# Kernel optimization log

Measured on AMD Instinct MI355X. Metric: run time of the kernel, lower is better.

## Reference

```python
import jax, jax.numpy as jnp
import numpy as np

B, S, E, H, L, V = 4, 1024, 256, 512, 16, 8000


def setup_inputs() -> dict:
    key = jax.random.key(0)
    ks = jax.random.split(key, 8)
    return {
        "sent": jax.random.randint(ks[0], (B, S), 0, V),
        "mask": jax.random.randint(ks[1], (B, S), 0, 2),
        "char_emb_w": jax.random.normal(ks[2], (V, E), dtype=jnp.float32) * 0.02,
        "mask_emb_w": jax.random.normal(ks[3], (2, E), dtype=jnp.float32) * 0.02,
        "wA": jax.random.normal(ks[4], (E, H), dtype=jnp.float32) * (1.0 / np.sqrt(E)),
        "bA": jnp.zeros((H,), dtype=jnp.float32),
        "wB": jax.random.normal(ks[5], (E, H), dtype=jnp.float32) * (1.0 / np.sqrt(E)),
        "bB": jnp.zeros((H,), dtype=jnp.float32),
        "wS": jax.random.normal(ks[6], (E, L), dtype=jnp.float32) * (1.0 / np.sqrt(E)),
        "bS": jnp.zeros((L,), dtype=jnp.float32),
    }


def reference(sent, mask, char_emb_w, mask_emb_w, wA, bA, wB, bB, wS, bS):
    # Embedding lookups: (B,S,E)
    ce = char_emb_w[sent]
    me = mask_emb_w[mask]
    # vemb = char_emb * GELU(mask_emb)  (torch GELU default = exact erf form)
    vemb = ce * jax.nn.gelu(me, approximate=False)
    va = vemb @ wA + bA                      # (B,S,H)
    vb = jax.nn.sigmoid(vemb @ wB + bB)      # (B,S,H)
    vc = jnp.einsum("bih,bjh->bij", va, vb) / H   # (B,S,S), biaffine score
    vd = jax.nn.relu(vemb @ wS + bS)         # (B,S,L)
    # torch: matmul(vc.unsqueeze(3), vd.unsqueeze(2)) -> (B,S,S,L) rank-1 outer product
    pred = jax.nn.softmax(vc[..., None] * vd[:, :, None, :], axis=-1)
    return pred
```

## Files before the change

kernel.cpp:

```cpp
#include <hip/hip_runtime.h>
#include <hip/hip_bf16.h>
#include <math.h>

typedef __attribute__((ext_vector_type(8))) short short8;
typedef __attribute__((ext_vector_type(4))) float f32x4;
typedef unsigned short u16;

#define Sn 1024
#define En 256
#define Hn 512
#define Ln 16

__device__ inline u16 bf16b(float x) {
    union { __hip_bfloat16 h; u16 u; } cvt;
    cvt.h = __float2bfloat16(x);
    return cvt.u;
}

__global__ void prep_embed(const float* __restrict__ wA, const float* __restrict__ wB,
                           const float* __restrict__ wS, u16* __restrict__ Wt,
                           const int* __restrict__ sent, const int* __restrict__ mask,
                           const float* __restrict__ ce_w, const float* __restrict__ me_w,
                           u16* __restrict__ vemb) {
    int bx = blockIdx.x;
    if (bx < 1088) {
        int idx = bx * 256 + threadIdx.x;
        int n = idx >> 8;
        int k = idx & 255;
        float v = 0.f;
        if (n < 512)       v = wA[k * 512 + n];
        else if (n < 1024) v = wB[k * 512 + (n - 512)];
        else if (n < 1040) v = wS[k * 16 + (n - 1024)];
        Wt[idx] = bf16b(v);
    } else {
        int row = bx - 1088;
        int e = threadIdx.x;
        int s = sent[row];
        int m = mask[row];
        float ce = ce_w[s * En + e];
        float me = me_w[m * En + e];
        float g = 0.5f * me * (1.f + erff(me * 0.70710678118654752f));
        vemb[row * En + e] = bf16b(ce * g);
    }
}

#define LDP 136
__global__ __launch_bounds__(256, 2) void gemm1(const u16* __restrict__ A, const u16* __restrict__ Bt,
                                                const float* __restrict__ bA, const float* __restrict__ bB,
                                                const float* __restrict__ bS,
                                                u16* __restrict__ va, u16* __restrict__ vb,
                                                float* __restrict__ vd,
                                                float* __restrict__ dmn, float* __restrict__ dmx) {
    __shared__ __align__(16) u16 As[64 * LDP];
    __shared__ __align__(16) u16 Bs[64 * LDP];
    int tid = threadIdx.x;
    int m0 = blockIdx.x * 64, n0 = blockIdx.y * 64;
    int lane = tid & 63, w = tid >> 6;
    int lrow = lane & 15, quad = lane >> 4;

    f32x4 acc[4];
    for (int nt = 0; nt < 4; nt++) acc[nt] = (f32x4){0.f, 0.f, 0.f, 0.f};

    for (int kb = 0; kb < 2; kb++) {
        for (int i = 0; i < 4; i++) {
            int off = (i * 256 + tid) * 8;
            int r = off >> 7, c = off & 127;
            *(short8*)&As[r * LDP + c] = *(const short8*)&A[(m0 + r) * 256 + kb * 128 + c];
            *(short8*)&Bs[r * LDP + c] = *(const short8*)&Bt[(n0 + r) * 256 + kb * 128 + c];
        }
        __syncthreads();
        for (int ks = 0; ks < 4; ks++) {
            short8 a = *(const short8*)&As[(w * 16 + lrow) * LDP + ks * 32 + quad * 8];
            for (int nt = 0; nt < 4; nt++) {
                short8 b = *(const short8*)&Bs[(nt * 16 + lrow) * LDP + ks * 32 + quad * 8];
                acc[nt] = __builtin_amdgcn_mfma_f32_16x16x32_bf16(a, b, acc[nt], 0, 0, 0);
            }
        }
        __syncthreads();
    }
    int mbase = m0 + w * 16 + quad * 4;
    if (blockIdx.y < 8) {
        for (int nt = 0; nt < 4; nt++) {
            int n = n0 + nt * 16 + lrow;
            float bias = bA[n];
            for (int r = 0; r < 4; r++)
                va[(mbase + r) * 512 + n] = bf16b(acc[nt][r] + bias);
        }
    } else if (blockIdx.y < 16) {
        for (int nt = 0; nt < 4; nt++) {
            int n = n0 + nt * 16 + lrow - 512;
            float bias = bB[n];
            for (int r = 0; r < 4; r++) {
                float x = acc[nt][r] + bias;
                vb[(mbase + r) * 512 + n] = bf16b(1.f / (1.f + __expf(-x)));
            }
        }
    } else {
        float bias = bS[lrow];
        for (int r = 0; r < 4; r++) {
            float x = acc[0][r] + bias;
            x = x > 0.f ? x : 0.f;
            vd[(mbase + r) * 16 + lrow] = x;
            float mn = x, mx = x;
            for (int d = 1; d < 16; d <<= 1) {
                mn = fminf(mn, __shfl_xor(mn, d));
                mx = fmaxf(mx, __shfl_xor(mx, d));
            }
            if (lrow == 0) {
                dmn[mbase + r] = mn;
                dmx[mbase + r] = mx;
            }
        }
    }
}

__global__ __launch_bounds__(256, 2) void gemm2(const u16* __restrict__ va_g, const u16* __restrict__ vb_g,
                                                float* __restrict__ vc) {
    __shared__ __align__(16) u16 As[64 * LDP];
    __shared__ __align__(16) u16 Bs[64 * LDP];
    int tid = threadIdx.x;
    int b = blockIdx.z;
    int m0 = blockIdx.x * 64, n0 = blockIdx.y * 64;
    const u16* A  = va_g + (size_t)b * 1024 * 512;
    const u16* Bt = vb_g + (size_t)b * 1024 * 512;
    int lane = tid & 63, w = tid >> 6;
    int lrow = lane & 15, quad = lane >> 4;

    f32x4 acc[4];
    for (int nt = 0; nt < 4; nt++) acc[nt] = (f32x4){0.f, 0.f, 0.f, 0.f};

    for (int kb = 0; kb < 4; kb++) {
        for (int i = 0; i < 4; i++) {
            int off = (i * 256 + tid) * 8;
            int r = off >> 7, c = off & 127;
            *(short8*)&As[r * LDP + c] = *(const short8*)&A[(m0 + r) * 512 + kb * 128 + c];
            *(short8*)&Bs[r * LDP + c] = *(const short8*)&Bt[(n0 + r) * 512 + kb * 128 + c];
        }
        __syncthreads();
        for (int ks = 0; ks < 4; ks++) {
            short8 a = *(const short8*)&As[(w * 16 + lrow) * LDP + ks * 32 + quad * 8];
            for (int nt = 0; nt < 4; nt++) {
                short8 bfr = *(const short8*)&Bs[(nt * 16 + lrow) * LDP + ks * 32 + quad * 8];
                acc[nt] = __builtin_amdgcn_mfma_f32_16x16x32_bf16(a, bfr, acc[nt], 0, 0, 0);
            }
        }
        __syncthreads();
    }
    const float invH = 1.0f / 512.0f;
    float* C = vc + (size_t)b * 1024 * 1024;
    int mbase = m0 + w * 16 + quad * 4;
    for (int nt = 0; nt < 4; nt++) {
        int n = n0 + nt * 16 + lrow;
        for (int r = 0; r < 4; r++)
            C[(mbase + r) * 1024 + n] = acc[nt][r] * invH;
    }
}

__global__ __launch_bounds__(256) void expand(const float* __restrict__ vc, const float* __restrict__ vd,
                                              const float* __restrict__ dmn, const float* __restrict__ dmx,
                                              float* __restrict__ out) {
    int gid = blockIdx.x * 256 + threadIdx.x;
    int t = gid & 3;
    int grp = gid >> 2;
    int j = grp & 1023;
    int bi = grp >> 10;
    int b = bi >> 10;
    float c = __builtin_nontemporal_load(&vc[grp]);
    int rowd = b * 1024 + j;
    f32x4 d = *(const f32x4*)&vd[rowd * 16 + t * 4];
    float m = (c >= 0.f) ? c * dmx[rowd] : c * dmn[rowd];
    float e0 = __expf(c * d.x - m);
    float e1 = __expf(c * d.y - m);
    float e2 = __expf(c * d.z - m);
    float e3 = __expf(c * d.w - m);
    float s = e0 + e1 + e2 + e3;
    s += __shfl_xor(s, 1);
    s += __shfl_xor(s, 2);
    float inv = 1.f / s;
    f32x4 o;
    o.x = e0 * inv; o.y = e1 * inv; o.z = e2 * inv; o.w = e3 * inv;
    __builtin_nontemporal_store(o, (f32x4*)&out[(size_t)grp * 16 + t * 4]);
}

extern "C" void kernel_launch(void* const* d_in, const int* in_sizes, int n_in,
                              void* d_out, int out_size, void* d_ws, size_t ws_size,
                              hipStream_t stream) {
    const int*   sent = (const int*)d_in[0];
    const int*   mask = (const int*)d_in[1];
    const float* ce_w = (const float*)d_in[2];
    const float* me_w = (const float*)d_in[3];
    const float* wA   = (const float*)d_in[4];
    const float* bA   = (const float*)d_in[5];
    const float* wB   = (const float*)d_in[6];
    const float* bB   = (const float*)d_in[7];
    const float* wS   = (const float*)d_in[8];
    const float* bS   = (const float*)d_in[9];
    float* out = (float*)d_out;

    char* ws = (char*)d_ws;
    u16* vemb = (u16*)ws;  ws += (size_t)4096 * 256 * 2;
    u16* Wt   = (u16*)ws;  ws += (size_t)1088 * 256 * 2;
    u16* va   = (u16*)ws;  ws += (size_t)4096 * 512 * 2;
    u16* vb   = (u16*)ws;  ws += (size_t)4096 * 512 * 2;
    float* vd  = (float*)ws;  ws += (size_t)4096 * 16 * 4;
    float* dmn = (float*)ws;  ws += (size_t)4096 * 4;
    float* dmx = (float*)ws;  ws += (size_t)4096 * 4;
    float* vc  = (float*)ws;  ws += (size_t)4 * 1024 * 1024 * 4;

    prep_embed<<<5184, 256, 0, stream>>>(wA, wB, wS, Wt, sent, mask, ce_w, me_w, vemb);
    gemm1<<<dim3(64, 17), 256, 0, stream>>>(vemb, Wt, bA, bB, bS, va, vb, vd, dmn, dmx);
    gemm2<<<dim3(16, 16, 4), 256, 0, stream>>>(va, vb, vc);
    expand<<<65536, 256, 0, stream>>>(vc, vd, dmn, dmx, out);
}
```

Measured before the change: 306.3 us.

## Fuse biaffine GEMM with rank-1 softmax expansion via shared-memory tile

The second GEMM now stages its 64x64 score tile in shared memory, reusing the operand buffers, and each block writes the softmax-expanded output for that tile directly. This removes the separate expand kernel and the 16 MB round trip of the fp32 score matrix through global memory. The trade-off is a longer GEMM epilogue: only 1024 blocks write the 256 MB output, so there is less parallelism for the store-bound phase than the old 65536-block expand kernel had.

```diff
diff --git a/kernel.cpp b/kernel.cpp
--- a/kernel.cpp
+++ b/kernel.cpp
@@ -114,10 +114,17 @@
     }
 }
 
-__global__ __launch_bounds__(256, 2) void gemm2(const u16* __restrict__ va_g, const u16* __restrict__ vb_g,
-                                                float* __restrict__ vc) {
-    __shared__ __align__(16) u16 As[64 * LDP];
-    __shared__ __align__(16) u16 Bs[64 * LDP];
+__global__ __launch_bounds__(256, 2) void gemm2_softmax(const u16* __restrict__ va_g,
+                                                        const u16* __restrict__ vb_g,
+                                                        const float* __restrict__ vd,
+                                                        const float* __restrict__ dmn,
+                                                        const float* __restrict__ dmx,
+                                                        float* __restrict__ out) {
+    __shared__ __align__(16) u16 smem[2 * 64 * LDP];
+    u16* As = smem;
+    u16* Bs = smem + 64 * LDP;
+    float* vcs = (float*)smem;
+
     int tid = threadIdx.x;
     int b = blockIdx.z;
     int m0 = blockIdx.x * 64, n0 = blockIdx.y * 64;
@@ -146,40 +153,37 @@
         }
         __syncthreads();
     }
+
     const float invH = 1.0f / 512.0f;
-    float* C = vc + (size_t)b * 1024 * 1024;
-    int mbase = m0 + w * 16 + quad * 4;
+    int rbase = w * 16 + quad * 4;
     for (int nt = 0; nt < 4; nt++) {
-        int n = n0 + nt * 16 + lrow;
+        int cl = nt * 16 + lrow;
         for (int r = 0; r < 4; r++)
-            C[(mbase + r) * 1024 + n] = acc[nt][r] * invH;
-    }
-}
-
-__global__ __launch_bounds__(256) void expand(const float* __restrict__ vc, const float* __restrict__ vd,
-                                              const float* __restrict__ dmn, const float* __restrict__ dmx,
-                                              float* __restrict__ out) {
-    int gid = blockIdx.x * 256 + threadIdx.x;
-    int t = gid & 3;
-    int grp = gid >> 2;
-    int j = grp & 1023;
-    int bi = grp >> 10;
-    int b = bi >> 10;
-    float c = __builtin_nontemporal_load(&vc[grp]);
-    int rowd = b * 1024 + j;
-    f32x4 d = *(const f32x4*)&vd[rowd * 16 + t * 4];
-    float m = (c >= 0.f) ? c * dmx[rowd] : c * dmn[rowd];
-    float e0 = __expf(c * d.x - m);
-    float e1 = __expf(c * d.y - m);
-    float e2 = __expf(c * d.z - m);
-    float e3 = __expf(c * d.w - m);
-    float s = e0 + e1 + e2 + e3;
-    s += __shfl_xor(s, 1);
-    s += __shfl_xor(s, 2);
-    float inv = 1.f / s;
-    f32x4 o;
-    o.x = e0 * inv; o.y = e1 * inv; o.z = e2 * inv; o.w = e3 * inv;
-    __builtin_nontemporal_store(o, (f32x4*)&out[(size_t)grp * 16 + t * 4]);
+            vcs[(rbase + r) * 65 + cl] = acc[nt][r] * invH;
+    }
+    __syncthreads();
+
+    int jl = tid >> 2;
+    int t4 = (tid & 3) * 4;
+    int rowd = b * 1024 + n0 + jl;
+    f32x4 d = *(const f32x4*)&vd[rowd * 16 + t4];
+    float mn = dmn[rowd], mx = dmx[rowd];
+    float* obase = out + (((size_t)(b * 1024 + m0) * 1024 + n0 + jl) * 16 + t4);
+    for (int il = 0; il < 64; il++) {
+        float c = vcs[il * 65 + jl];
+        float mval = (c >= 0.f) ? c * mx : c * mn;
+        float e0 = __expf(c * d.x - mval);
+        float e1 = __expf(c * d.y - mval);
+        float e2 = __expf(c * d.z - mval);
+        float e3 = __expf(c * d.w - mval);
+        float s = e0 + e1 + e2 + e3;
+        s += __shfl_xor(s, 1);
+        s += __shfl_xor(s, 2);
+        float inv = 1.f / s;
+        f32x4 o;
+        o.x = e0 * inv; o.y = e1 * inv; o.z = e2 * inv; o.w = e3 * inv;
+        __builtin_nontemporal_store(o, (f32x4*)(obase + (size_t)il * 1024 * 16));
+    }
 }
 
 extern "C" void kernel_launch(void* const* d_in, const int* in_sizes, int n_in,
@@ -205,10 +209,8 @@
     float* vd  = (float*)ws;  ws += (size_t)4096 * 16 * 4;
     float* dmn = (float*)ws;  ws += (size_t)4096 * 4;
     float* dmx = (float*)ws;  ws += (size_t)4096 * 4;
-    float* vc  = (float*)ws;  ws += (size_t)4 * 1024 * 1024 * 4;
 
     prep_embed<<<5184, 256, 0, stream>>>(wA, wB, wS, Wt, sent, mask, ce_w, me_w, vemb);
     gemm1<<<dim3(64, 17), 256, 0, stream>>>(vemb, Wt, bA, bB, bS, va, vb, vd, dmn, dmx);
-    gemm2<<<dim3(16, 16, 4), 256, 0, stream>>>(va, vb, vc);
-    expand<<<65536, 256, 0, stream>>>(vc, vd, dmn, dmx, out);
-}
+    gemm2_softmax<<<dim3(16, 16, 4), 256, 0, stream>>>(va, vb, vd, dmn, dmx, out);
+}
```

Result: no change. 308.3 us (+0.7%).

## Retile biaffine GEMM to 128x128 per block and store scores as bf16

Applied to the files above, without the earlier changes.

The batched va·vbᵀ GEMM moves from 64x64 tiles with a 128-wide K step to 128x128 tiles with a 64-wide K step. Each wave now computes a 64x64 sub-tile with a 4x4 MFMA accumulator grid, which raises fragment reuse and cuts global/LDS traffic per FLOP. The intermediate score matrix vc is written in bf16 and widened in the expand kernel, halving its write and read traffic. The cost is more accumulator registers, fewer blocks (256), and lower precision of the scores that feed the softmax.

```diff
diff --git a/kernel.cpp b/kernel.cpp
--- a/kernel.cpp
+++ b/kernel.cpp
@@ -15,6 +15,12 @@
     union { __hip_bfloat16 h; u16 u; } cvt;
     cvt.h = __float2bfloat16(x);
     return cvt.u;
+}
+
+__device__ inline float b2f(u16 u) {
+    union { unsigned int i; float f; } cvt;
+    cvt.i = ((unsigned int)u) << 16;
+    return cvt.f;
 }
 
 __global__ void prep_embed(const float* __restrict__ wA, const float* __restrict__ wB,
@@ -114,49 +120,58 @@
     }
 }
 
+#define LDB 72
 __global__ __launch_bounds__(256, 2) void gemm2(const u16* __restrict__ va_g, const u16* __restrict__ vb_g,
-                                                float* __restrict__ vc) {
-    __shared__ __align__(16) u16 As[64 * LDP];
-    __shared__ __align__(16) u16 Bs[64 * LDP];
+                                                u16* __restrict__ vc) {
+    __shared__ __align__(16) u16 As[128 * LDB];
+    __shared__ __align__(16) u16 Bs[128 * LDB];
     int tid = threadIdx.x;
     int b = blockIdx.z;
-    int m0 = blockIdx.x * 64, n0 = blockIdx.y * 64;
+    int m0 = blockIdx.x * 128, n0 = blockIdx.y * 128;
     const u16* A  = va_g + (size_t)b * 1024 * 512;
     const u16* Bt = vb_g + (size_t)b * 1024 * 512;
     int lane = tid & 63, w = tid >> 6;
+    int wr = (w & 1) * 64, wc = (w >> 1) * 64;
     int lrow = lane & 15, quad = lane >> 4;
 
-    f32x4 acc[4];
-    for (int nt = 0; nt < 4; nt++) acc[nt] = (f32x4){0.f, 0.f, 0.f, 0.f};
-
-    for (int kb = 0; kb < 4; kb++) {
+    f32x4 acc[4][4];
+    for (int mt = 0; mt < 4; mt++)
+        for (int nt = 0; nt < 4; nt++)
+            acc[mt][nt] = (f32x4){0.f, 0.f, 0.f, 0.f};
+
+    for (int kb = 0; kb < 8; kb++) {
         for (int i = 0; i < 4; i++) {
-            int off = (i * 256 + tid) * 8;
-            int r = off >> 7, c = off & 127;
-            *(short8*)&As[r * LDP + c] = *(const short8*)&A[(m0 + r) * 512 + kb * 128 + c];
-            *(short8*)&Bs[r * LDP + c] = *(const short8*)&Bt[(n0 + r) * 512 + kb * 128 + c];
-        }
-        __syncthreads();
-        for (int ks = 0; ks < 4; ks++) {
-            short8 a = *(const short8*)&As[(w * 16 + lrow) * LDP + ks * 32 + quad * 8];
-            for (int nt = 0; nt < 4; nt++) {
-                short8 bfr = *(const short8*)&Bs[(nt * 16 + lrow) * LDP + ks * 32 + quad * 8];
-                acc[nt] = __builtin_amdgcn_mfma_f32_16x16x32_bf16(a, bfr, acc[nt], 0, 0, 0);
-            }
+            int v = i * 256 + tid;
+            int r = v >> 3, c8 = (v & 7) * 8;
+            *(short8*)&As[r * LDB + c8] = *(const short8*)&A[(m0 + r) * 512 + kb * 64 + c8];
+            *(short8*)&Bs[r * LDB + c8] = *(const short8*)&Bt[(n0 + r) * 512 + kb * 64 + c8];
+        }
+        __syncthreads();
+        for (int ks = 0; ks < 2; ks++) {
+            short8 af[4], bf[4];
+            for (int mt = 0; mt < 4; mt++)
+                af[mt] = *(const short8*)&As[(wr + mt * 16 + lrow) * LDB + ks * 32 + quad * 8];
+            for (int nt = 0; nt < 4; nt++)
+                bf[nt] = *(const short8*)&Bs[(wc + nt * 16 + lrow) * LDB + ks * 32 + quad * 8];
+            for (int mt = 0; mt < 4; mt++)
+                for (int nt = 0; nt < 4; nt++)
+                    acc[mt][nt] = __builtin_amdgcn_mfma_f32_16x16x32_bf16(af[mt], bf[nt], acc[mt][nt], 0, 0, 0);
         }
         __syncthreads();
     }
     const float invH = 1.0f / 512.0f;
-    float* C = vc + (size_t)b * 1024 * 1024;
-    int mbase = m0 + w * 16 + quad * 4;
-    for (int nt = 0; nt < 4; nt++) {
-        int n = n0 + nt * 16 + lrow;
-        for (int r = 0; r < 4; r++)
-            C[(mbase + r) * 1024 + n] = acc[nt][r] * invH;
-    }
-}
-
-__global__ __launch_bounds__(256) void expand(const float* __restrict__ vc, const float* __restrict__ vd,
+    u16* C = vc + (size_t)b * 1024 * 1024;
+    for (int mt = 0; mt < 4; mt++) {
+        int mm = m0 + wr + mt * 16 + quad * 4;
+        for (int nt = 0; nt < 4; nt++) {
+            int n = n0 + wc + nt * 16 + lrow;
+            for (int r = 0; r < 4; r++)
+                C[(size_t)(mm + r) * 1024 + n] = bf16b(acc[mt][nt][r] * invH);
+        }
+    }
+}
+
+__global__ __launch_bounds__(256) void expand(const u16* __restrict__ vc, const float* __restrict__ vd,
                                               const float* __restrict__ dmn, const float* __restrict__ dmx,
                                               float* __restrict__ out) {
     int gid = blockIdx.x * 256 + threadIdx.x;
@@ -165,7 +180,7 @@
     int j = grp & 1023;
     int bi = grp >> 10;
     int b = bi >> 10;
-    float c = __builtin_nontemporal_load(&vc[grp]);
+    float c = b2f(__builtin_nontemporal_load(&vc[grp]));
     int rowd = b * 1024 + j;
     f32x4 d = *(const f32x4*)&vd[rowd * 16 + t * 4];
     float m = (c >= 0.f) ? c * dmx[rowd] : c * dmn[rowd];
@@ -205,10 +220,10 @@
     float* vd  = (float*)ws;  ws += (size_t)4096 * 16 * 4;
     float* dmn = (float*)ws;  ws += (size_t)4096 * 4;
     float* dmx = (float*)ws;  ws += (size_t)4096 * 4;
-    float* vc  = (float*)ws;  ws += (size_t)4 * 1024 * 1024 * 4;
+    u16* vc   = (u16*)ws;  ws += (size_t)4 * 1024 * 1024 * 2;
 
     prep_embed<<<5184, 256, 0, stream>>>(wA, wB, wS, Wt, sent, mask, ce_w, me_w, vemb);
     gemm1<<<dim3(64, 17), 256, 0, stream>>>(vemb, Wt, bA, bB, bS, va, vb, vd, dmn, dmx);
-    gemm2<<<dim3(16, 16, 4), 256, 0, stream>>>(va, vb, vc);
+    gemm2<<<dim3(8, 8, 4), 256, 0, stream>>>(va, vb, vc);
     expand<<<65536, 256, 0, stream>>>(vc, vd, dmn, dmx, out);
 }
```

Result: slower. 319.3 us (+4.3%).
